# Performance work log

Measured on AMD Instinct MI355X. Metric: run time of the kernel, lower is better.

Reference implementation:

```python
import jax, jax.numpy as jnp
import numpy as np

B, S, D_MODEL, H = 4, 1025, 1024, 16
DEPTH = D_MODEL // H
LEAKY_ALPHA = 0.2  # tf.nn.leaky_relu default
NEG_INF = -1e9


def _dense_params(key, d_in, d_out):
    kw, kb = jax.random.split(key)
    W = jax.random.normal(kw, (d_in, d_out), dtype=jnp.float32) * 0.02
    b = jnp.zeros((d_out,), dtype=jnp.float32)
    return W, b


def setup_inputs() -> dict:
    key = jax.random.key(0)
    ks = jax.random.split(key, 13)
    inp = {
        'q': jax.random.normal(ks[0], (B, S, D_MODEL), dtype=jnp.float32),
        'k': jax.random.normal(ks[1], (B, S, D_MODEL), dtype=jnp.float32),
        'v': jax.random.normal(ks[2], (B, S - 1, D_MODEL), dtype=jnp.float32),
        'e': jax.random.normal(ks[3], (B, S, D_MODEL), dtype=jnp.float32),
        'mask': jax.random.randint(ks[4], (B, S - 1, S - 1), 0, 2).astype(jnp.float32),
    }
    names = ['wq', 'wq2', 'wq3', 'wk', 'wk2', 'wk3', 'wv', 'wo']
    for i, nm in enumerate(names):
        W, b = _dense_params(ks[5 + i], D_MODEL, D_MODEL)
        inp['W' + nm] = W
        inp['b' + nm] = b
    return inp


def _split_heads(x):
    # (B, S, d_model) -> (B, H, S, depth)
    b, s, _ = x.shape
    return x.reshape(b, s, H, DEPTH).transpose(0, 2, 1, 3)


def reference(q, k, v, e, mask,
              Wwq, bwq, Wwq2, bwq2, Wwq3, bwq3,
              Wwk, bwk, Wwk2, bwk2, Wwk3, bwk3,
              Wwv, bwv, Wwo, bwo):
    # Q/K pre-projections mixed with edge/extra features e, leaky_relu(alpha=0.2)
    qp = jax.nn.leaky_relu(q @ Wwq + bwq + e @ Wwq2 + bwq2, LEAKY_ALPHA) @ Wwq3 + bwq3
    kp = jax.nn.leaky_relu(k @ Wwk + bwk + e @ Wwk2 + bwk2, LEAKY_ALPHA) @ Wwk3 + bwk3
    vp = v @ Wwv + bwv

    qh = _split_heads(qp)  # (B,H,S,depth)
    kh = _split_heads(kp)  # (B,H,S,depth)
    vh = _split_heads(vp)  # (B,H,S-1,depth)

    # scores: (B,H,S,S) then slice rows 1: and cols :-1 -> (B,H,S-1,S-1)
    scores = jnp.einsum('bhqd,bhkd->bhqk', qh, kh)
    sliced = scores[:, :, 1:, :-1]
    scale = 1.0 / jnp.sqrt(jnp.asarray(DEPTH, dtype=sliced.dtype))
    nl_qk = jax.nn.relu(sliced * scale) + mask[:, None, :, :] * NEG_INF
    att_weights = jax.nn.softmax(nl_qk, axis=-1)  # (B,H,S-1,S-1)

    out = jnp.einsum('bhqk,bhkd->bhqd', att_weights, vh)  # (B,H,S-1,depth)
    out = out.transpose(0, 2, 1, 3).reshape(out.shape[0], -1, D_MODEL)
    output = out @ Wwo + bwo  # (B,S-1,d_model)
    return output, att_weights
```

## Files before the change

### kernel.cpp

```cpp
#include <hip/hip_runtime.h>

#define DM 1024
typedef unsigned short u16;
typedef __attribute__((ext_vector_type(8))) short short8;
typedef __attribute__((ext_vector_type(4))) float f32x4;

__device__ __forceinline__ float4 ldg4(const float* p) {
    return *reinterpret_cast<const float4*>(p);
}

__device__ __forceinline__ void split2(float x, u16& hi, u16& lo) {
    unsigned u = __float_as_uint(x);
    hi = (u16)(u >> 16);
    float hif = __uint_as_float(u & 0xffff0000u);
    lo = (u16)(__float_as_uint(x - hif) >> 16);
}

__device__ __forceinline__ u16 bf16rn(float x) {
    unsigned u = __float_as_uint(x);
    return (u16)((u + 0x7fffu + ((u >> 16) & 1u)) >> 16);
}

__device__ __forceinline__ int swzc(int row, int col) {
    return (col & ~63) | (((((col >> 3) & 7) ^ (row & 7))) << 3) | (col & 7);
}

__device__ __forceinline__ void gl_lds16(const u16* g, u16* l) {
    __builtin_amdgcn_global_load_lds(
        (const __attribute__((address_space(1))) void*)g,
        (__attribute__((address_space(3))) void*)l, 16, 0, 0);
}

struct PJob { const float* src; int astride, aoff; u16* dh; u16* dl; };
struct PJobs { PJob j[5]; };

__global__ __launch_bounds__(256) void prep_k(PJobs js) {
    const PJob J = js.j[blockIdx.x >> 12];
    const int row = blockIdx.x & 4095;
    const int t = threadIdx.x;
    const size_t srow = (size_t)(row >> 10) * J.astride + (row & 1023) + J.aoff;
    float4 v = ldg4(J.src + srow * DM + t * 4);
    u16 h[4], l[4];
    split2(v.x, h[0], l[0]); split2(v.y, h[1], l[1]);
    split2(v.z, h[2], l[2]); split2(v.w, h[3], l[3]);
    ushort4 h4 = {h[0], h[1], h[2], h[3]};
    ushort4 l4 = {l[0], l[1], l[2], l[3]};
    const int c = swzc(row, t * 4);
    *reinterpret_cast<ushort4*>(J.dh + (size_t)row * DM + c) = h4;
    *reinterpret_cast<ushort4*>(J.dl + (size_t)row * DM + c) = l4;
}

struct WPack {
    const float* in[8];
    u16* hi[8];
    u16* lo[8];
};

__global__ __launch_bounds__(256) void convw_k(WPack p) {
    __shared__ float T[32][33];
    const int w = blockIdx.y;
    const int tr = blockIdx.x >> 5, tc = blockIdx.x & 31;
    const int t = threadIdx.x;
    {
        int lr = t >> 3, c4 = t & 7;
        float4 v = ldg4(p.in[w] + (size_t)(tr * 32 + lr) * DM + tc * 32 + c4 * 4);
        T[lr][c4 * 4 + 0] = v.x; T[lr][c4 * 4 + 1] = v.y;
        T[lr][c4 * 4 + 2] = v.z; T[lr][c4 * 4 + 3] = v.w;
    }
    __syncthreads();
    const int n = tc * 32 + (t >> 3);
    const int kb = tr * 32 + (t & 7) * 4;
    ushort4 h4, l4;
    u16 hh, ll;
    split2(T[(t & 7) * 4 + 0][t >> 3], hh, ll); h4.x = hh; l4.x = ll;
    split2(T[(t & 7) * 4 + 1][t >> 3], hh, ll); h4.y = hh; l4.y = ll;
    split2(T[(t & 7) * 4 + 2][t >> 3], hh, ll); h4.z = hh; l4.z = ll;
    split2(T[(t & 7) * 4 + 3][t >> 3], hh, ll); h4.w = hh; l4.w = ll;
    const int c = swzc(n, kb);
    *reinterpret_cast<ushort4*>(p.hi[w] + (size_t)n * DM + c) = h4;
    *reinterpret_cast<ushort4*>(p.lo[w] + (size_t)n * DM + c) = l4;
}

struct GJob {
    const u16 *Ah, *Al, *A2h, *A2l;
    const u16 *Bh, *Bl, *B2h, *B2l;
    const float *b1, *b2;
    float* Cf; u16 *Ch; u16 *Cl;
    int nt, act, outsplit, dualk;
};
struct GJobs { GJob j[3]; };

__global__ __launch_bounds__(256) void gemm5(GJobs js) {
    extern __shared__ u16 lds[];
    const GJob J = js.j[blockIdx.x >> 8];
    const int bid = blockIdx.x & 255;
    const int t = threadIdx.x;
    const int bm = bid >> 3, bn = bid & 7;
    const int lane = t & 63, w = t >> 6;
    const int wm = w >> 1, wn = w & 1;
    const int fr = lane & 15, fq = lane >> 4;

    const size_t ga = ((size_t)(bm * 128 + w * 32 + (lane >> 3))) * DM + (lane & 7) * 8;
    const size_t gb = ((size_t)(bn * 128 + w * 32 + (lane >> 3))) * DM + (lane & 7) * 8;

    f32x4 acc[4][4];
    #pragma unroll
    for (int i = 0; i < 4; ++i)
        #pragma unroll
        for (int j = 0; j < 4; ++j)
            acc[i][j] = (f32x4){0.f, 0.f, 0.f, 0.f};

    const int NT = J.nt;
    for (int kt = 0; kt < NT; ++kt) {
        const bool second = J.dualk && (kt >= 16);
        const int ekt = J.dualk ? (kt & 15) : kt;
        const u16* pAh = second ? J.A2h : J.Ah;
        const u16* pAl = second ? J.A2l : J.Al;
        const u16* pBh = second ? J.B2h : J.Bh;
        const u16* pBl = second ? J.B2l : J.Bl;
        const size_t ka = ga + ekt * 64;
        const size_t kb = gb + ekt * 64;

        __syncthreads();
        #pragma unroll
        for (int i = 0; i < 4; ++i) {
            const int lo = w * 2048 + i * 512;
            const size_t go = (size_t)i * 8 * DM;
            gl_lds16(pAh + ka + go, lds +         lo);
            gl_lds16(pAl + ka + go, lds +  8192 + lo);
            gl_lds16(pBh + kb + go, lds + 16384 + lo);
            gl_lds16(pBl + kb + go, lds + 24576 + lo);
        }
        __syncthreads();

        #pragma unroll
        for (int kk = 0; kk < 2; ++kk) {
            short8 ah[4], al[4];
            #pragma unroll
            for (int mi = 0; mi < 4; ++mi) {
                const int row = wm * 64 + mi * 16 + fr;
                const int off = row * 64 + (((kk * 4 + fq) ^ (row & 7)) << 3);
                ah[mi] = *reinterpret_cast<const short8*>(lds + off);
                al[mi] = *reinterpret_cast<const short8*>(lds + 8192 + off);
            }
            #pragma unroll
            for (int nj = 0; nj < 4; ++nj) {
                const int rb = wn * 64 + nj * 16 + fr;
                const int off = rb * 64 + (((kk * 4 + fq) ^ (rb & 7)) << 3);
                short8 bh = *reinterpret_cast<const short8*>(lds + 16384 + off);
                short8 bl = *reinterpret_cast<const short8*>(lds + 24576 + off);
                #pragma unroll
                for (int mi = 0; mi < 4; ++mi) {
                    acc[mi][nj] = __builtin_amdgcn_mfma_f32_16x16x32_bf16(ah[mi], bh, acc[mi][nj], 0, 0, 0);
                    acc[mi][nj] = __builtin_amdgcn_mfma_f32_16x16x32_bf16(ah[mi], bl, acc[mi][nj], 0, 0, 0);
                    acc[mi][nj] = __builtin_amdgcn_mfma_f32_16x16x32_bf16(al[mi], bh, acc[mi][nj], 0, 0, 0);
                }
            }
        }
    }

    #pragma unroll
    for (int nj = 0; nj < 4; ++nj) {
        const int col = bn * 128 + wn * 64 + nj * 16 + fr;
        float bv = J.b1[col];
        if (J.dualk) bv += J.b2[col];
        #pragma unroll
        for (int mi = 0; mi < 4; ++mi) {
            const int row0 = bm * 128 + wm * 64 + mi * 16 + fq * 4;
            #pragma unroll
            for (int rr = 0; rr < 4; ++rr) {
                float x = acc[mi][nj][rr] + bv;
                if (J.act) x = (x >= 0.f) ? x : 0.2f * x;
                const int row = row0 + rr;
                if (J.outsplit) {
                    u16 hh, ll;
                    split2(x, hh, ll);
                    const size_t off = (size_t)row * DM + swzc(row, col);
                    J.Ch[off] = hh;
                    J.Cl[off] = ll;
                } else {
                    J.Cf[(size_t)row * DM + col] = x;
                }
            }
        }
    }
}

__global__ __launch_bounds__(256) void attn2(
    const float* __restrict__ qp, const float* __restrict__ kp,
    const float* __restrict__ vp, const float* __restrict__ mask,
    float* __restrict__ att, u16* __restrict__ omidH, u16* __restrict__ omidL,
    float* __restrict__ rsg)
{
    extern __shared__ u16 sm16[];
    u16* Qh  = sm16;
    u16* Ql  = sm16 + 4608;
    u16* Kh  = sm16 + 9216;
    u16* Kl  = sm16 + 18432;
    float* Sf = (float*)(sm16 + 9216);
    u16* Vth = sm16 + 9216;
    u16* Vtl = sm16 + 17920;
    u16* Ps  = sm16 + 27648;
    float* rs = (float*)(sm16 + 36352);

    const int t = threadIdx.x;
    const int lane = t & 63, w = t >> 6;
    const int wm = w >> 1, wn = w & 1;
    const int fr = lane & 15, fq = lane >> 4;
    const int blk = blockIdx.x;
    const int qt = blk & 15, hh = (blk >> 4) & 15, b = blk >> 8;
    const int q0 = qt * 64;

    const size_t qbase  = ((size_t)b * 1024 + q0) * DM + hh * 64;
    const size_t kvbase = ((size_t)b * 1024) * DM + hh * 64;
    const size_t mbase  = ((size_t)b) << 20;
    const size_t abase  = ((size_t)(b * 16 + hh)) << 20;

    #pragma unroll
    for (int l = 0; l < 4; ++l) {
        int f = t + l * 256;
        int r = f >> 4, dq = f & 15;
        float4 v = ldg4(qp + qbase + (size_t)r * DM + dq * 4);
        u16 hi, lo; ushort4 h4, l4;
        split2(v.x, hi, lo); h4.x = hi; l4.x = lo;
        split2(v.y, hi, lo); h4.y = hi; l4.y = lo;
        split2(v.z, hi, lo); h4.z = hi; l4.z = lo;
        split2(v.w, hi, lo); h4.w = hi; l4.w = lo;
        *reinterpret_cast<ushort4*>(Qh + r * 72 + dq * 4) = h4;
        *reinterpret_cast<ushort4*>(Ql + r * 72 + dq * 4) = l4;
    }

    f32x4 pv[2][2];
    #pragma unroll
    for (int i = 0; i < 2; ++i)
        #pragma unroll
        for (int j = 0; j < 2; ++j)
            pv[i][j] = (f32x4){0.f, 0.f, 0.f, 0.f};
    float rpart[8] = {};

    for (int kt2 = 0; kt2 < 8; ++kt2) {
        const int kb = kt2 * 128;
        __syncthreads();

        #pragma unroll
        for (int l = 0; l < 8; ++l) {
            int f = t + l * 256;
            int r = f >> 4, dq = f & 15;
            float4 v = ldg4(kp + kvbase + (size_t)(kb + r) * DM + dq * 4);
            u16 hi, lo; ushort4 h4, l4;
            split2(v.x, hi, lo); h4.x = hi; l4.x = lo;
            split2(v.y, hi, lo); h4.y = hi; l4.y = lo;
            split2(v.z, hi, lo); h4.z = hi; l4.z = lo;
            split2(v.w, hi, lo); h4.w = hi; l4.w = lo;
            *reinterpret_cast<ushort4*>(Kh + r * 72 + dq * 4) = h4;
            *reinterpret_cast<ushort4*>(Kl + r * 72 + dq * 4) = l4;
        }
        __syncthreads();

        f32x4 accs[2][4];
        #pragma unroll
        for (int i = 0; i < 2; ++i)
            #pragma unroll
            for (int j = 0; j < 4; ++j)
                accs[i][j] = (f32x4){0.f, 0.f, 0.f, 0.f};
        #pragma unroll
        for (int kk = 0; kk < 2; ++kk) {
            short8 qh_[2], ql_[2];
            #pragma unroll
            for (int mi = 0; mi < 2; ++mi) {
                const int off = (wm * 32 + mi * 16 + fr) * 72 + kk * 32 + fq * 8;
                qh_[mi] = *reinterpret_cast<const short8*>(Qh + off);
                ql_[mi] = *reinterpret_cast<const short8*>(Ql + off);
            }
            #pragma unroll
            for (int nj = 0; nj < 4; ++nj) {
                const int off = (wn * 64 + nj * 16 + fr) * 72 + kk * 32 + fq * 8;
                short8 kh_ = *reinterpret_cast<const short8*>(Kh + off);
                short8 kl_ = *reinterpret_cast<const short8*>(Kl + off);
                #pragma unroll
                for (int mi = 0; mi < 2; ++mi) {
                    accs[mi][nj] = __builtin_amdgcn_mfma_f32_16x16x32_bf16(qh_[mi], kh_, accs[mi][nj], 0, 0, 0);
                    accs[mi][nj] = __builtin_amdgcn_mfma_f32_16x16x32_bf16(qh_[mi], kl_, accs[mi][nj], 0, 0, 0);
                    accs[mi][nj] = __builtin_amdgcn_mfma_f32_16x16x32_bf16(ql_[mi], kh_, accs[mi][nj], 0, 0, 0);
                }
            }
        }
        __syncthreads();

        #pragma unroll
        for (int mi = 0; mi < 2; ++mi)
            #pragma unroll
            for (int rr = 0; rr < 4; ++rr) {
                const int qrow = wm * 32 + mi * 16 + fq * 4 + rr;
                #pragma unroll
                for (int nj = 0; nj < 4; ++nj)
                    Sf[qrow * 132 + wn * 64 + nj * 16 + fr] = accs[mi][nj][rr];
            }
        __syncthreads();

        #pragma unroll
        for (int l = 0; l < 8; ++l) {
            const int row = (t >> 5) + l * 8;
            const int gq = q0 + row;
            float4 sv = *reinterpret_cast<const float4*>(Sf + row * 132 + (t & 31) * 4);
            float4 mv = ldg4(mask + mbase + (size_t)gq * 1024 + kb + (t & 31) * 4);
            float e[4];
            float s4[4] = {sv.x, sv.y, sv.z, sv.w};
            float m4[4] = {mv.x, mv.y, mv.z, mv.w};
            #pragma unroll
            for (int u = 0; u < 4; ++u) {
                float x = fmaxf(s4[u] * 0.125f, 0.f);
                x = fmaf(m4[u], -1.0e9f, x);
                e[u] = __expf(x);
                rpart[l] += e[u];
            }
            float4 ev = {e[0], e[1], e[2], e[3]};
            *reinterpret_cast<float4*>(att + abase + (size_t)gq * 1024 + kb + (t & 31) * 4) = ev;
            ushort4 pp = {bf16rn(e[0]), bf16rn(e[1]), bf16rn(e[2]), bf16rn(e[3])};
            *reinterpret_cast<ushort4*>(Ps + row * 136 + (t & 31) * 4) = pp;
        }
        __syncthreads();

        {
            const int k_ = t >> 1, hd = t & 1;
            const float* src = vp + kvbase + (size_t)(kb + k_) * DM + hd * 32;
            #pragma unroll
            for (int c = 0; c < 8; ++c) {
                float4 v = ldg4(src + c * 4);
                const int d0 = hd * 32 + c * 4;
                u16 hi, lo;
                split2(v.x, hi, lo); Vth[(d0+0)*136 + k_] = hi; Vtl[(d0+0)*136 + k_] = lo;
                split2(v.y, hi, lo); Vth[(d0+1)*136 + k_] = hi; Vtl[(d0+1)*136 + k_] = lo;
                split2(v.z, hi, lo); Vth[(d0+2)*136 + k_] = hi; Vtl[(d0+2)*136 + k_] = lo;
                split2(v.w, hi, lo); Vth[(d0+3)*136 + k_] = hi; Vtl[(d0+3)*136 + k_] = lo;
            }
        }
        __syncthreads();

        #pragma unroll
        for (int kk = 0; kk < 4; ++kk) {
            short8 pa[2];
            #pragma unroll
            for (int mi = 0; mi < 2; ++mi)
                pa[mi] = *reinterpret_cast<const short8*>(
                    Ps + (wm * 32 + mi * 16 + fr) * 136 + kk * 32 + fq * 8);
            #pragma unroll
            for (int nj = 0; nj < 2; ++nj) {
                const int off = (wn * 32 + nj * 16 + fr) * 136 + kk * 32 + fq * 8;
                short8 vh_ = *reinterpret_cast<const short8*>(Vth + off);
                short8 vl_ = *reinterpret_cast<const short8*>(Vtl + off);
                #pragma unroll
                for (int mi = 0; mi < 2; ++mi) {
                    pv[mi][nj] = __builtin_amdgcn_mfma_f32_16x16x32_bf16(pa[mi], vh_, pv[mi][nj], 0, 0, 0);
                    pv[mi][nj] = __builtin_amdgcn_mfma_f32_16x16x32_bf16(pa[mi], vl_, pv[mi][nj], 0, 0, 0);
                }
            }
        }
    }

    #pragma unroll
    for (int l = 0; l < 8; ++l) {
        float v = rpart[l];
        v += __shfl_xor(v, 1);
        v += __shfl_xor(v, 2);
        v += __shfl_xor(v, 4);
        v += __shfl_xor(v, 8);
        v += __shfl_xor(v, 16);
        if ((t & 31) == 0) rs[(t >> 5) + l * 8] = v;
    }
    __syncthreads();
    if (t < 64) {
        float iv = 1.f / rs[t];
        rs[t] = iv;
        rsg[(size_t)(b * 16 + hh) * 1024 + q0 + t] = iv;
    }
    __syncthreads();

    #pragma unroll
    for (int mi = 0; mi < 2; ++mi) {
        #pragma unroll
        for (int rr = 0; rr < 4; ++rr) {
            const int qrow = wm * 32 + mi * 16 + fq * 4 + rr;
            const float iv = rs[qrow];
            const size_t grow = (size_t)b * 1024 + q0 + qrow;
            #pragma unroll
            for (int nj = 0; nj < 2; ++nj) {
                const int d = hh * 64 + wn * 32 + nj * 16 + fr;
                float x = pv[mi][nj][rr] * iv;
                u16 hi, lo;
                split2(x, hi, lo);
                const size_t off = grow * DM + swzc(qrow, d);
                omidH[off] = hi;
                omidL[off] = lo;
            }
        }
    }
}

__global__ __launch_bounds__(256) void norm_k(
    float* __restrict__ att, const float* __restrict__ rsg)
{
    const size_t total = (size_t)67108864 / 4;
    for (size_t i = (size_t)blockIdx.x * 256 + threadIdx.x; i < total;
         i += (size_t)gridDim.x * 256) {
        float4 v = reinterpret_cast<float4*>(att)[i];
        float s = rsg[i >> 8];
        v.x *= s; v.y *= s; v.z *= s; v.w *= s;
        reinterpret_cast<float4*>(att)[i] = v;
    }
}

extern "C" void kernel_launch(void* const* d_in, const int* in_sizes, int n_in,
                              void* d_out, int out_size, void* d_ws, size_t ws_size,
                              hipStream_t stream)
{
    const float* q    = (const float*)d_in[0];
    const float* k    = (const float*)d_in[1];
    const float* v    = (const float*)d_in[2];
    const float* e    = (const float*)d_in[3];
    const float* mask = (const float*)d_in[4];
    const float* bq   = (const float*)d_in[6];
    const float* bq2  = (const float*)d_in[8];
    const float* bq3  = (const float*)d_in[10];
    const float* bk   = (const float*)d_in[12];
    const float* bk2  = (const float*)d_in[14];
    const float* bk3  = (const float*)d_in[16];
    const float* bv   = (const float*)d_in[18];
    const float* bo   = (const float*)d_in[20];

    float* out = (float*)d_out;
    float* att = out + (size_t)4096 * 1024;

    u16* WT = (u16*)d_ws;
    const size_t WSZ = 1048576;
    const size_t NA = (size_t)4096 * 1024;
    float* qp   = (float*)(WT + 16 * WSZ);
    float* kp   = qp + NA;
    float* vpp  = kp + NA;
    u16* omidH  = (u16*)(vpp + NA);
    u16* omidL  = omidH + NA;
    float* rsg  = (float*)(omidL + NA);

    u16* AR   = (u16*)att;
    u16* QspH = AR;            u16* QspL = QspH + NA;
    u16* E1H  = QspL + NA;     u16* E1L  = E1H + NA;
    u16* KspH = E1L + NA;      u16* KspL = KspH + NA;
    u16* E0H  = KspL + NA;     u16* E0L  = E0H + NA;
    u16* VsH  = E0L + NA;      u16* VsL  = VsH + NA;
    u16* tQH  = VsL + NA;      u16* tQL  = tQH + NA;
    u16* tKH  = tQL + NA;      u16* tKL  = tKH + NA;

    PJobs pj;
    pj.j[0] = PJob{q, 1025, 1, QspH, QspL};
    pj.j[1] = PJob{e, 1025, 1, E1H, E1L};
    pj.j[2] = PJob{k, 1025, 0, KspH, KspL};
    pj.j[3] = PJob{e, 1025, 0, E0H, E0L};
    pj.j[4] = PJob{v, 1024, 0, VsH, VsL};
    prep_k<<<dim3(5 * 4096), 256, 0, stream>>>(pj);

    WPack wp;
    #pragma unroll
    for (int i = 0; i < 8; ++i) {
        wp.in[i] = (const float*)d_in[5 + 2 * i];
        wp.hi[i] = WT + (size_t)i * 2 * WSZ;
        wp.lo[i] = WT + (size_t)i * 2 * WSZ + WSZ;
    }
    convw_k<<<dim3(1024, 8), 256, 0, stream>>>(wp);

    hipFuncSetAttribute((const void*)gemm5, hipFuncAttributeMaxDynamicSharedMemorySize, 65536);

    GJobs JA;
    JA.j[0] = GJob{QspH, QspL, E1H, E1L, wp.hi[0], wp.lo[0], wp.hi[1], wp.lo[1],
                   bq, bq2, nullptr, tQH, tQL, 32, 1, 1, 1};
    JA.j[1] = GJob{KspH, KspL, E0H, E0L, wp.hi[3], wp.lo[3], wp.hi[4], wp.lo[4],
                   bk, bk2, nullptr, tKH, tKL, 32, 1, 1, 1};
    JA.j[2] = GJob{VsH, VsL, nullptr, nullptr, wp.hi[6], wp.lo[6], nullptr, nullptr,
                   bv, nullptr, vpp, nullptr, nullptr, 16, 0, 0, 0};
    gemm5<<<dim3(768), 256, 65536, stream>>>(JA);

    GJobs JB;
    JB.j[0] = GJob{tQH, tQL, nullptr, nullptr, wp.hi[2], wp.lo[2], nullptr, nullptr,
                   bq3, nullptr, qp, nullptr, nullptr, 16, 0, 0, 0};
    JB.j[1] = GJob{tKH, tKL, nullptr, nullptr, wp.hi[5], wp.lo[5], nullptr, nullptr,
                   bk3, nullptr, kp, nullptr, nullptr, 16, 0, 0, 0};
    JB.j[2] = JB.j[0];
    gemm5<<<dim3(512), 256, 65536, stream>>>(JB);

    const int smemA = 72960;
    hipFuncSetAttribute((const void*)attn2, hipFuncAttributeMaxDynamicSharedMemorySize, smemA);
    attn2<<<dim3(1024), 256, smemA, stream>>>(qp, kp, vpp, mask, att, omidH, omidL, rsg);

    norm_k<<<dim3(16384), 256, 0, stream>>>(att, rsg);

    GJobs JC;
    JC.j[0] = GJob{omidH, omidL, nullptr, nullptr, wp.hi[7], wp.lo[7], nullptr, nullptr,
                   bo, nullptr, out, nullptr, nullptr, 16, 0, 0, 0};
    JC.j[1] = JC.j[0];
    JC.j[2] = JC.j[0];
    gemm5<<<dim3(256), 256, 65536, stream>>>(JC);
}
```

Measured before the change: 857.5 us.

## Double-buffer GEMM LDS tiles, remap block order, prefetch K/V/mask in attention

The GEMM kernel gets two LDS stages, so the next k-tile's global-to-LDS load is issued before the current tile's MFMAs, with one barrier per iteration instead of two. Its block index is also remapped so consecutive blocks walk down M instead of across N, which changes cache locality. The attention kernel prefetches the next K tile, plus the current V and mask tiles, into registers so their latency overlaps the score MFMAs. This doubles GEMM LDS use to 128 KB, which may limit it to one block per CU, and adds register pressure in attention.

```diff
diff --git a/kernel.cpp b/kernel.cpp
--- a/kernel.cpp
+++ b/kernel.cpp
@@ -90,10 +90,11 @@
 };
 struct GJobs { GJob j[3]; };
 
-__global__ __launch_bounds__(256) void gemm5(GJobs js) {
+__global__ __launch_bounds__(256) void gemm6(GJobs js) {
     extern __shared__ u16 lds[];
     const GJob J = js.j[blockIdx.x >> 8];
-    const int bid = blockIdx.x & 255;
+    const int lb = blockIdx.x & 255;
+    const int bid = ((lb & 7) << 5) | (lb >> 3);
     const int t = threadIdx.x;
     const int bm = bid >> 3, bn = bid & 7;
     const int lane = t & 63, w = t >> 6;
@@ -110,8 +111,7 @@
         for (int j = 0; j < 4; ++j)
             acc[i][j] = (f32x4){0.f, 0.f, 0.f, 0.f};
 
-    const int NT = J.nt;
-    for (int kt = 0; kt < NT; ++kt) {
+    auto STAGE = [&](int kt, int buf) {
         const bool second = J.dualk && (kt >= 16);
         const int ekt = J.dualk ? (kt & 15) : kt;
         const u16* pAh = second ? J.A2h : J.Ah;
@@ -120,19 +120,20 @@
         const u16* pBl = second ? J.B2l : J.Bl;
         const size_t ka = ga + ekt * 64;
         const size_t kb = gb + ekt * 64;
-
-        __syncthreads();
+        u16* base = lds + buf * 32768;
         #pragma unroll
         for (int i = 0; i < 4; ++i) {
             const int lo = w * 2048 + i * 512;
             const size_t go = (size_t)i * 8 * DM;
-            gl_lds16(pAh + ka + go, lds +         lo);
-            gl_lds16(pAl + ka + go, lds +  8192 + lo);
-            gl_lds16(pBh + kb + go, lds + 16384 + lo);
-            gl_lds16(pBl + kb + go, lds + 24576 + lo);
-        }
-        __syncthreads();
-
+            gl_lds16(pAh + ka + go, base +         lo);
+            gl_lds16(pAl + ka + go, base +  8192 + lo);
+            gl_lds16(pBh + kb + go, base + 16384 + lo);
+            gl_lds16(pBl + kb + go, base + 24576 + lo);
+        }
+    };
+
+    auto COMPUTE = [&](int buf) {
+        const u16* base = lds + buf * 32768;
         #pragma unroll
         for (int kk = 0; kk < 2; ++kk) {
             short8 ah[4], al[4];
@@ -140,15 +141,15 @@
             for (int mi = 0; mi < 4; ++mi) {
                 const int row = wm * 64 + mi * 16 + fr;
                 const int off = row * 64 + (((kk * 4 + fq) ^ (row & 7)) << 3);
-                ah[mi] = *reinterpret_cast<const short8*>(lds + off);
-                al[mi] = *reinterpret_cast<const short8*>(lds + 8192 + off);
+                ah[mi] = *reinterpret_cast<const short8*>(base + off);
+                al[mi] = *reinterpret_cast<const short8*>(base + 8192 + off);
             }
             #pragma unroll
             for (int nj = 0; nj < 4; ++nj) {
                 const int rb = wn * 64 + nj * 16 + fr;
                 const int off = rb * 64 + (((kk * 4 + fq) ^ (rb & 7)) << 3);
-                short8 bh = *reinterpret_cast<const short8*>(lds + 16384 + off);
-                short8 bl = *reinterpret_cast<const short8*>(lds + 24576 + off);
+                short8 bh = *reinterpret_cast<const short8*>(base + 16384 + off);
+                short8 bl = *reinterpret_cast<const short8*>(base + 24576 + off);
                 #pragma unroll
                 for (int mi = 0; mi < 4; ++mi) {
                     acc[mi][nj] = __builtin_amdgcn_mfma_f32_16x16x32_bf16(ah[mi], bh, acc[mi][nj], 0, 0, 0);
@@ -157,6 +158,15 @@
                 }
             }
         }
+    };
+
+    const int NT = J.nt;
+    STAGE(0, 0);
+    __syncthreads();
+    for (int kt = 0; kt < NT; ++kt) {
+        if (kt + 1 < NT) STAGE(kt + 1, (kt + 1) & 1);
+        COMPUTE(kt & 1);
+        __syncthreads();
     }
 
     #pragma unroll
@@ -238,6 +248,14 @@
             pv[i][j] = (f32x4){0.f, 0.f, 0.f, 0.f};
     float rpart[8] = {};
 
+    float4 kreg[8];
+    #pragma unroll
+    for (int l = 0; l < 8; ++l) {
+        int f = t + l * 256;
+        int r = f >> 4, dq = f & 15;
+        kreg[l] = ldg4(kp + kvbase + (size_t)r * DM + dq * 4);
+    }
+
     for (int kt2 = 0; kt2 < 8; ++kt2) {
         const int kb = kt2 * 128;
         __syncthreads();
@@ -246,7 +264,7 @@
         for (int l = 0; l < 8; ++l) {
             int f = t + l * 256;
             int r = f >> 4, dq = f & 15;
-            float4 v = ldg4(kp + kvbase + (size_t)(kb + r) * DM + dq * 4);
+            float4 v = kreg[l];
             u16 hi, lo; ushort4 h4, l4;
             split2(v.x, hi, lo); h4.x = hi; l4.x = lo;
             split2(v.y, hi, lo); h4.y = hi; l4.y = lo;
@@ -256,6 +274,19 @@
             *reinterpret_cast<ushort4*>(Kl + r * 72 + dq * 4) = l4;
         }
         __syncthreads();
+
+        float4 vreg[8], mreg[8];
+        {
+            const int k_ = t >> 1, hd = t & 1;
+            const float* src = vp + kvbase + (size_t)(kb + k_) * DM + hd * 32;
+            #pragma unroll
+            for (int c = 0; c < 8; ++c) vreg[c] = ldg4(src + c * 4);
+        }
+        #pragma unroll
+        for (int l = 0; l < 8; ++l) {
+            const int row = (t >> 5) + l * 8;
+            mreg[l] = ldg4(mask + mbase + (size_t)(q0 + row) * 1024 + kb + (t & 31) * 4);
+        }
 
         f32x4 accs[2][4];
         #pragma unroll
@@ -303,10 +334,9 @@
             const int row = (t >> 5) + l * 8;
             const int gq = q0 + row;
             float4 sv = *reinterpret_cast<const float4*>(Sf + row * 132 + (t & 31) * 4);
-            float4 mv = ldg4(mask + mbase + (size_t)gq * 1024 + kb + (t & 31) * 4);
             float e[4];
             float s4[4] = {sv.x, sv.y, sv.z, sv.w};
-            float m4[4] = {mv.x, mv.y, mv.z, mv.w};
+            float m4[4] = {mreg[l].x, mreg[l].y, mreg[l].z, mreg[l].w};
             #pragma unroll
             for (int u = 0; u < 4; ++u) {
                 float x = fmaxf(s4[u] * 0.125f, 0.f);
@@ -323,10 +353,9 @@
 
         {
             const int k_ = t >> 1, hd = t & 1;
-            const float* src = vp + kvbase + (size_t)(kb + k_) * DM + hd * 32;
             #pragma unroll
             for (int c = 0; c < 8; ++c) {
-                float4 v = ldg4(src + c * 4);
+                float4 v = vreg[c];
                 const int d0 = hd * 32 + c * 4;
                 u16 hi, lo;
                 split2(v.x, hi, lo); Vth[(d0+0)*136 + k_] = hi; Vtl[(d0+0)*136 + k_] = lo;
@@ -336,6 +365,16 @@
             }
         }
         __syncthreads();
+
+        {
+            const int nkb = (kt2 < 7 ? kt2 + 1 : 7) * 128;
+            #pragma unroll
+            for (int l = 0; l < 8; ++l) {
+                int f = t + l * 256;
+                int r = f >> 4, dq = f & 15;
+                kreg[l] = ldg4(kp + kvbase + (size_t)(nkb + r) * DM + dq * 4);
+            }
+        }
 
         #pragma unroll
         for (int kk = 0; kk < 4; ++kk) {
@@ -467,7 +506,7 @@
     }
     convw_k<<<dim3(1024, 8), 256, 0, stream>>>(wp);
 
-    hipFuncSetAttribute((const void*)gemm5, hipFuncAttributeMaxDynamicSharedMemorySize, 65536);
+    hipFuncSetAttribute((const void*)gemm6, hipFuncAttributeMaxDynamicSharedMemorySize, 131072);
 
     GJobs JA;
     JA.j[0] = GJob{QspH, QspL, E1H, E1L, wp.hi[0], wp.lo[0], wp.hi[1], wp.lo[1],
@@ -476,7 +515,7 @@
                    bk, bk2, nullptr, tKH, tKL, 32, 1, 1, 1};
     JA.j[2] = GJob{VsH, VsL, nullptr, nullptr, wp.hi[6], wp.lo[6], nullptr, nullptr,
                    bv, nullptr, vpp, nullptr, nullptr, 16, 0, 0, 0};
-    gemm5<<<dim3(768), 256, 65536, stream>>>(JA);
+    gemm6<<<dim3(768), 256, 131072, stream>>>(JA);
 
     GJobs JB;
     JB.j[0] = GJob{tQH, tQL, nullptr, nullptr, wp.hi[2], wp.lo[2], nullptr, nullptr,
@@ -484,7 +523,7 @@
     JB.j[1] = GJob{tKH, tKL, nullptr, nullptr, wp.hi[5], wp.lo[5], nullptr, nullptr,
                    bk3, nullptr, kp, nullptr, nullptr, 16, 0, 0, 0};
     JB.j[2] = JB.j[0];
-    gemm5<<<dim3(512), 256, 65536, stream>>>(JB);
+    gemm6<<<dim3(512), 256, 131072, stream>>>(JB);
 
     const int smemA = 72960;
     hipFuncSetAttribute((const void*)attn2, hipFuncAttributeMaxDynamicSharedMemorySize, smemA);
@@ -497,5 +536,5 @@
                    bo, nullptr, out, nullptr, nullptr, 16, 0, 0, 0};
     JC.j[1] = JC.j[0];
     JC.j[2] = JC.j[0];
-    gemm5<<<dim3(256), 256, 65536, stream>>>(JC);
-}
+    gemm6<<<dim3(256), 256, 131072, stream>>>(JC);
+}
```

Measured after the change: 823.6 us. -4.0%, faster.
